# Kernel tuning notes

Hardware: AMD Instinct MI355X
Metric: run time of the kernel (lower is better)

## Reference

```python
import jax, jax.numpy as jnp
import numpy as np


def setup_inputs() -> dict:
    key = jax.random.key(0)
    k1, k2, k3 = jax.random.split(key, 3)
    l, p, m, n = 8, 1, 4096, 1024
    inp = jax.random.normal(k1, (l, p, m, n), dtype=jnp.float32)
    alpha = jax.random.uniform(k2, (1,), dtype=jnp.float32, minval=0.001, maxval=1.0)
    beta = jax.random.uniform(k3, (1,), dtype=jnp.float32, minval=0.001, maxval=1.0)
    return {"input": inp, "alpha": alpha, "beta": beta}


def reference(input, alpha, beta):
    # w[0] = 1; w[k] = w[k-1] + alpha / w[k-1] - beta * input[..., k-1]
    l, p, m, n = input.shape
    a = alpha[0]
    b = beta[0]
    # scan over the last axis: move it to leading axis; only first n-1 inputs drive the recurrence
    xs = jnp.moveaxis(input[..., : n - 1], -1, 0)  # (n-1, l, p, m)
    w0 = jnp.ones((l, p, m), dtype=input.dtype)

    def step(w, x):
        w_next = w + a / w - b * x
        return w_next, w_next

    _, ws = jax.lax.scan(step, w0, xs)  # (n-1, l, p, m)
    wm = jnp.concatenate([w0[None], ws], axis=0)  # (n, l, p, m)
    wm = jnp.moveaxis(wm, 0, -1)  # (l, p, m, n)
    return wm.reshape(l, m * n)  # valid because p == 1
```

## Files before the change

kernel.cpp:

```cpp
#include <hip/hip_runtime.h>


#define N_COLS 1024
#define CHUNK 16

__device__ __forceinline__ float stepf(float w, float x, float a, float b) {
    return __fsub_rn(__fadd_rn(w, __fdiv_rn(a, w)), __fmul_rn(b, x));
}

__device__ __forceinline__ void load_chunk(const float4* __restrict__ p, int j,
                                           float* __restrict__ x) {
#pragma unroll
    for (int q = 0; q < CHUNK / 4; ++q) {
        float4 t = p[j * (CHUNK / 4) + q];
        x[q * 4 + 0] = t.x;
        x[q * 4 + 1] = t.y;
        x[q * 4 + 2] = t.z;
        x[q * 4 + 3] = t.w;
    }
}

__device__ __forceinline__ void store_chunk(float4* __restrict__ p, int j,
                                            const float* __restrict__ o) {
#pragma unroll
    for (int q = 0; q < CHUNK / 4; ++q) {
        float4 t;
        t.x = o[q * 4 + 0];
        t.y = o[q * 4 + 1];
        t.z = o[q * 4 + 2];
        t.w = o[q * 4 + 3];
        p[j * (CHUNK / 4) + q] = t;
    }
}

__global__ __launch_bounds__(64) void DDK_77644418777662_kernel(
    const float* __restrict__ in, float* __restrict__ out,
    const float* __restrict__ alpha, const float* __restrict__ beta,
    int n_rows) {
    int row = blockIdx.x * 64 + threadIdx.x;
    if (row >= n_rows) return;

    const float a = alpha[0];
    const float b = beta[0];

    const float4* __restrict__ inr =
        reinterpret_cast<const float4*>(in + (size_t)row * N_COLS);
    float4* __restrict__ outr =
        reinterpret_cast<float4*>(out + (size_t)row * N_COLS);

    constexpr int NC = N_COLS / CHUNK;

    float x[CHUNK], xn[CHUNK], o[CHUNK];
    float w = 1.0f;

    load_chunk(inr, 0, x);

#pragma unroll 2
    for (int j = 0; j < NC; ++j) {
        if (j + 1 < NC) load_chunk(inr, j + 1, xn);

        o[0] = w;
#pragma unroll
        for (int i = 1; i < CHUNK; ++i) {
            w = stepf(w, x[i - 1], a, b);
            o[i] = w;
        }
        w = stepf(w, x[CHUNK - 1], a, b);

        store_chunk(outr, j, o);

#pragma unroll
        for (int i = 0; i < CHUNK; ++i) x[i] = xn[i];
    }
}

extern "C" void kernel_launch(void* const* d_in, const int* in_sizes, int n_in,
                              void* d_out, int out_size, void* d_ws, size_t ws_size,
                              hipStream_t stream) {
    const float* in = (const float*)d_in[0];
    const float* alpha = (const float*)d_in[1];
    const float* beta = (const float*)d_in[2];
    float* out = (float*)d_out;

    int total = in_sizes[0];
    int n_rows = total / N_COLS;

    dim3 grid((n_rows + 63) / 64);
    dim3 block(64);
    DDK_77644418777662_kernel<<<grid, block, 0, stream>>>(in, out, alpha, beta,
                                                          n_rows);
}
```

Baseline: 308.8 us.

## Stage input through LDS with async global_load_lds ring buffer and manual vmcnt waits

Replaces per-thread strided float4 global loads with a cooperative, coalesced global-to-LDS async copy (global_load_lds) into an 8-deep ring of chunk buffers. Each lane then reads its swizzled 16-element slice from LDS, while loads run 7 chunks ahead under hand-written s_waitcnt vmcnt counters. This targets the poor coalescing of row-per-thread reads and the latency exposure of the serial divide-bound recurrence. It relies on exact vmcnt bookkeeping, which also counts the output stores, and on no barrier being needed within a single wave. Any miscount would give a race.

```diff
diff --git a/kernel.cpp b/kernel.cpp
--- a/kernel.cpp
+++ b/kernel.cpp
@@ -2,76 +2,113 @@
 
 
 #define N_COLS 1024
-#define CHUNK 16
+#define NCHUNK 64
+#define NBUF 8
+
+#define WAITVM(n) asm volatile("s_waitcnt vmcnt(" #n ")" ::: "memory")
+#define WAITLGKM0() asm volatile("s_waitcnt lgkmcnt(0)" ::: "memory")
 
 __device__ __forceinline__ float stepf(float w, float x, float a, float b) {
     return __fsub_rn(__fadd_rn(w, __fdiv_rn(a, w)), __fmul_rn(b, x));
-}
-
-__device__ __forceinline__ void load_chunk(const float4* __restrict__ p, int j,
-                                           float* __restrict__ x) {
-#pragma unroll
-    for (int q = 0; q < CHUNK / 4; ++q) {
-        float4 t = p[j * (CHUNK / 4) + q];
-        x[q * 4 + 0] = t.x;
-        x[q * 4 + 1] = t.y;
-        x[q * 4 + 2] = t.z;
-        x[q * 4 + 3] = t.w;
-    }
-}
-
-__device__ __forceinline__ void store_chunk(float4* __restrict__ p, int j,
-                                            const float* __restrict__ o) {
-#pragma unroll
-    for (int q = 0; q < CHUNK / 4; ++q) {
-        float4 t;
-        t.x = o[q * 4 + 0];
-        t.y = o[q * 4 + 1];
-        t.z = o[q * 4 + 2];
-        t.w = o[q * 4 + 3];
-        p[j * (CHUNK / 4) + q] = t;
-    }
 }
 
 __global__ __launch_bounds__(64) void DDK_77644418777662_kernel(
     const float* __restrict__ in, float* __restrict__ out,
     const float* __restrict__ alpha, const float* __restrict__ beta,
     int n_rows) {
-    int row = blockIdx.x * 64 + threadIdx.x;
-    if (row >= n_rows) return;
+    __shared__ float lds[NBUF * 1024];
+
+    const int lane = threadIdx.x;
+    const int row_base = blockIdx.x * 64;
+    if (row_base >= n_rows) return;
 
     const float a = alpha[0];
     const float b = beta[0];
+    asm volatile("s_waitcnt vmcnt(0) lgkmcnt(0)" ::: "memory");
 
-    const float4* __restrict__ inr =
-        reinterpret_cast<const float4*>(in + (size_t)row * N_COLS);
-    float4* __restrict__ outr =
-        reinterpret_cast<float4*>(out + (size_t)row * N_COLS);
+    const int t = lane >> 2;
+    const int u = lane & 3;
+    const int c4 = u ^ ((t >> 1) & 3);
+    const float* pb0 = in + (size_t)(row_base + t) * N_COLS + c4 * 4;
+    const float* pb1 = pb0 + 16 * N_COLS;
+    const float* pb2 = pb0 + 32 * N_COLS;
+    const float* pb3 = pb0 + 48 * N_COLS;
 
-    constexpr int NC = N_COLS / CHUNK;
+    const int s2 = (lane >> 1) & 3;
+    const int sbase = 64 * (lane >> 4) + 4 * (lane & 15);
+    const int sl0 = (sbase + (0 ^ s2)) * 4;
+    const int sl1 = (sbase + (1 ^ s2)) * 4;
+    const int sl2 = (sbase + (2 ^ s2)) * 4;
+    const int sl3 = (sbase + (3 ^ s2)) * 4;
 
-    float x[CHUNK], xn[CHUNK], o[CHUNK];
+    float* outp = out + (size_t)(row_base + lane) * N_COLS;
+
+#define STAGE(c) do {                                                          \
+    float* dst_ = &lds[((c) & 7) * 1024];                                      \
+    __builtin_amdgcn_global_load_lds(                                          \
+        (const __attribute__((address_space(1))) void*)(pb0 + (c) * 16),       \
+        (__attribute__((address_space(3))) void*)(dst_ + 0), 16, 0, 0);        \
+    __builtin_amdgcn_global_load_lds(                                          \
+        (const __attribute__((address_space(1))) void*)(pb1 + (c) * 16),       \
+        (__attribute__((address_space(3))) void*)(dst_ + 256), 16, 0, 0);      \
+    __builtin_amdgcn_global_load_lds(                                          \
+        (const __attribute__((address_space(1))) void*)(pb2 + (c) * 16),       \
+        (__attribute__((address_space(3))) void*)(dst_ + 512), 16, 0, 0);      \
+    __builtin_amdgcn_global_load_lds(                                          \
+        (const __attribute__((address_space(1))) void*)(pb3 + (c) * 16),       \
+        (__attribute__((address_space(3))) void*)(dst_ + 768), 16, 0, 0);      \
+} while (0)
+
     float w = 1.0f;
 
-    load_chunk(inr, 0, x);
+#define BODY(c, DO_LOAD) do {                                                  \
+    const float* bufp_ = &lds[((c) & 7) * 1024];                               \
+    float4 xa_ = *(const float4*)(bufp_ + sl0);                                \
+    float4 xb_ = *(const float4*)(bufp_ + sl1);                                \
+    float4 xc_ = *(const float4*)(bufp_ + sl2);                                \
+    float4 xd_ = *(const float4*)(bufp_ + sl3);                                \
+    WAITLGKM0();                                                               \
+    if (DO_LOAD) STAGE((c) + 7);                                               \
+    float x_[16] = {xa_.x, xa_.y, xa_.z, xa_.w, xb_.x, xb_.y, xb_.z, xb_.w,    \
+                    xc_.x, xc_.y, xc_.z, xc_.w, xd_.x, xd_.y, xd_.z, xd_.w};   \
+    float o_[16];                                                              \
+    o_[0] = w;                                                                 \
+    _Pragma("unroll")                                                          \
+    for (int i_ = 1; i_ < 16; ++i_) { w = stepf(w, x_[i_ - 1], a, b); o_[i_] = w; } \
+    w = stepf(w, x_[15], a, b);                                                \
+    float4* op_ = (float4*)(outp + (c) * 16);                                  \
+    op_[0] = make_float4(o_[0], o_[1], o_[2], o_[3]);                          \
+    op_[1] = make_float4(o_[4], o_[5], o_[6], o_[7]);                          \
+    op_[2] = make_float4(o_[8], o_[9], o_[10], o_[11]);                        \
+    op_[3] = make_float4(o_[12], o_[13], o_[14], o_[15]);                      \
+} while (0)
 
-#pragma unroll 2
-    for (int j = 0; j < NC; ++j) {
-        if (j + 1 < NC) load_chunk(inr, j + 1, xn);
+    STAGE(0); STAGE(1); STAGE(2); STAGE(3); STAGE(4); STAGE(5); STAGE(6);
 
-        o[0] = w;
-#pragma unroll
-        for (int i = 1; i < CHUNK; ++i) {
-            w = stepf(w, x[i - 1], a, b);
-            o[i] = w;
-        }
-        w = stepf(w, x[CHUNK - 1], a, b);
+    WAITVM(24); BODY(0, 1);
+    WAITVM(28); BODY(1, 1);
+    WAITVM(32); BODY(2, 1);
+    WAITVM(36); BODY(3, 1);
+    WAITVM(40); BODY(4, 1);
+    WAITVM(44); BODY(5, 1);
+    WAITVM(48); BODY(6, 1);
 
-        store_chunk(outr, j, o);
+#pragma unroll 1
+    for (int c = 7; c <= 56; ++c) {
+        WAITVM(52);
+        BODY(c, 1);
+    }
 
-#pragma unroll
-        for (int i = 0; i < CHUNK; ++i) x[i] = xn[i];
-    }
+    WAITVM(52); BODY(57, 0);
+    WAITVM(48); BODY(58, 0);
+    WAITVM(44); BODY(59, 0);
+    WAITVM(40); BODY(60, 0);
+    WAITVM(36); BODY(61, 0);
+    WAITVM(32); BODY(62, 0);
+    WAITVM(28); BODY(63, 0);
+
+#undef BODY
+#undef STAGE
 }
 
 extern "C" void kernel_launch(void* const* d_in, const int* in_sizes, int n_in,
```

Measured after the change: 307.1 us. About the same (-0.6%).

## Warp-specialize recurrence kernel with async LDS loader, compute and store waves

Applied to the files above, without the earlier changes.

Restructures each 256-thread block into a loader wave that stages 16-column chunks for 128 rows into a 6-deep LDS ring via global_load_lds, two compute waves that run the sequential recurrence from LDS, and a store wave that drains a double-buffered LDS output to global memory. The goal is to overlap memory traffic with the latency-bound per-row recurrence and to get coalesced, swizzled row-chunk accesses. It also replaces the compiler division with hand-written inline asm for the IEEE-correct divide sequence. In exchange it adds a block barrier on every chunk, leaves half the waves without arithmetic, and assumes n_rows is a multiple of 128.

```diff
diff --git a/kernel.cpp b/kernel.cpp
--- a/kernel.cpp
+++ b/kernel.cpp
@@ -2,75 +2,157 @@
 
 
 #define N_COLS 1024
-#define CHUNK 16
+#define NCHUNK 64
+#define KIN 6
+
+#define WAITVM(n) asm volatile("s_waitcnt vmcnt(" #n ")" ::: "memory")
+#define WAITLGKM0() asm volatile("s_waitcnt lgkmcnt(0)" ::: "memory")
+#define BARRIER() __builtin_amdgcn_s_barrier()
+
+__device__ __forceinline__ float fdiv_rn_exact(float a, float w) {
+    float d, n, r0, e, r1, q, e2, q1, e3, f, res;
+    unsigned long long sj;
+    asm volatile(
+        "v_div_scale_f32 %[d], vcc, %[w], %[w], %[a]\n\t"
+        "v_div_scale_f32 %[n], %[sj], %[a], %[w], %[a]\n\t"
+        "v_rcp_f32 %[r0], %[d]\n\t"
+        "s_nop 1\n\t"
+        "v_fma_f32 %[e], -%[d], %[r0], 1.0\n\t"
+        "v_fma_f32 %[r1], %[e], %[r0], %[r0]\n\t"
+        "v_mul_f32 %[q], %[n], %[r1]\n\t"
+        "v_fma_f32 %[e2], -%[d], %[q], %[n]\n\t"
+        "v_fma_f32 %[q1], %[e2], %[r1], %[q]\n\t"
+        "v_fma_f32 %[e3], -%[d], %[q1], %[n]\n\t"
+        "v_div_fmas_f32 %[f], %[e3], %[r1], %[q1]\n\t"
+        "v_div_fixup_f32 %[res], %[f], %[w], %[a]"
+        : [d] "=&v"(d), [n] "=&v"(n), [r0] "=&v"(r0), [e] "=&v"(e),
+          [r1] "=&v"(r1), [q] "=&v"(q), [e2] "=&v"(e2), [q1] "=&v"(q1),
+          [e3] "=&v"(e3), [f] "=&v"(f), [res] "=v"(res), [sj] "=&s"(sj)
+        : [a] "v"(a), [w] "v"(w)
+        : "vcc");
+    return res;
+}
 
 __device__ __forceinline__ float stepf(float w, float x, float a, float b) {
-    return __fsub_rn(__fadd_rn(w, __fdiv_rn(a, w)), __fmul_rn(b, x));
+    return __fsub_rn(__fadd_rn(w, fdiv_rn_exact(a, w)), __fmul_rn(b, x));
 }
 
-__device__ __forceinline__ void load_chunk(const float4* __restrict__ p, int j,
-                                           float* __restrict__ x) {
-#pragma unroll
-    for (int q = 0; q < CHUNK / 4; ++q) {
-        float4 t = p[j * (CHUNK / 4) + q];
-        x[q * 4 + 0] = t.x;
-        x[q * 4 + 1] = t.y;
-        x[q * 4 + 2] = t.z;
-        x[q * 4 + 3] = t.w;
-    }
-}
-
-__device__ __forceinline__ void store_chunk(float4* __restrict__ p, int j,
-                                            const float* __restrict__ o) {
-#pragma unroll
-    for (int q = 0; q < CHUNK / 4; ++q) {
-        float4 t;
-        t.x = o[q * 4 + 0];
-        t.y = o[q * 4 + 1];
-        t.z = o[q * 4 + 2];
-        t.w = o[q * 4 + 3];
-        p[j * (CHUNK / 4) + q] = t;
-    }
-}
-
-__global__ __launch_bounds__(64) void DDK_77644418777662_kernel(
+__global__ __launch_bounds__(256) void DDK_77644418777662_kernel(
     const float* __restrict__ in, float* __restrict__ out,
     const float* __restrict__ alpha, const float* __restrict__ beta,
     int n_rows) {
-    int row = blockIdx.x * 64 + threadIdx.x;
-    if (row >= n_rows) return;
+    __shared__ float ibuf[KIN * 2048];
+    __shared__ float obuf[2 * 2048];
 
-    const float a = alpha[0];
-    const float b = beta[0];
+    const int tid = threadIdx.x;
+    const int wid = tid >> 6;
+    const int lane = tid & 63;
+    const int row_base = blockIdx.x * 128;
+    if (row_base >= n_rows) return;
 
-    const float4* __restrict__ inr =
-        reinterpret_cast<const float4*>(in + (size_t)row * N_COLS);
-    float4* __restrict__ outr =
-        reinterpret_cast<float4*>(out + (size_t)row * N_COLS);
+    const int t = lane >> 2;
+    const int u = lane & 3;
+    const int cg = u ^ ((t >> 1) & 3);
 
-    constexpr int NC = N_COLS / CHUNK;
+    if (wid == 2) {
+        const float* src0 = in + (size_t)(row_base + t) * N_COLS + cg * 4;
 
-    float x[CHUNK], xn[CHUNK], o[CHUNK];
-    float w = 1.0f;
+#define STAGE_AT(S, C) do {                                                    \
+    float* dst_ = ibuf + (S) * 2048;                                           \
+    const float* s_ = src0 + (size_t)(C) * 16;                                 \
+    _Pragma("unroll")                                                          \
+    for (int q_ = 0; q_ < 8; ++q_) {                                           \
+        __builtin_amdgcn_global_load_lds(                                      \
+            (const __attribute__((address_space(1))) void*)(s_ + q_ * 16 * N_COLS), \
+            (__attribute__((address_space(3))) void*)(dst_ + q_ * 256), 16, 0, 0);  \
+    }                                                                          \
+} while (0)
 
-    load_chunk(inr, 0, x);
+        WAITVM(0);
+        STAGE_AT(0, 0); STAGE_AT(1, 1); STAGE_AT(2, 2);
+        STAGE_AT(3, 3); STAGE_AT(4, 4);
+        WAITVM(32);
 
-#pragma unroll 2
-    for (int j = 0; j < NC; ++j) {
-        if (j + 1 < NC) load_chunk(inr, j + 1, xn);
+        int slot = KIN - 1;
+#pragma unroll 1
+        for (int c = 0; c < NCHUNK; ++c) {
+            BARRIER();
+            if (c <= NCHUNK - KIN) {
+                STAGE_AT(slot, c + KIN - 1);
+                WAITVM(32);
+                if (++slot == KIN) slot = 0;
+            } else if (c == 59) { WAITVM(24); }
+            else if (c == 60) { WAITVM(16); }
+            else if (c == 61) { WAITVM(8); }
+            else if (c == 62) { WAITVM(0); }
+        }
+        BARRIER();
+#undef STAGE_AT
 
-        o[0] = w;
+    } else if (wid == 3) {
+        float* dst0 = out + (size_t)(row_base + t) * N_COLS + cg * 4;
+
+#define STORE_CHUNK(C) do {                                                    \
+    const float* ob_ = obuf + ((C) & 1) * 2048;                                \
+    float4 v_[8];                                                              \
+    _Pragma("unroll")                                                          \
+    for (int q_ = 0; q_ < 8; ++q_)                                             \
+        v_[q_] = *(const float4*)(ob_ + q_ * 256 + lane * 4);                  \
+    WAITLGKM0();                                                               \
+    _Pragma("unroll")                                                          \
+    for (int q_ = 0; q_ < 8; ++q_)                                             \
+        *(float4*)(dst0 + (size_t)q_ * 16 * N_COLS + (size_t)(C) * 16) = v_[q_]; \
+} while (0)
+
+#pragma unroll 1
+        for (int c = 0; c < NCHUNK; ++c) {
+            BARRIER();
+            if (c >= 1) STORE_CHUNK(c - 1);
+        }
+        BARRIER();
+        STORE_CHUNK(NCHUNK - 1);
+#undef STORE_CHUNK
+
+    } else {
+        const float a = alpha[0];
+        const float b = beta[0];
+
+        const int r = (wid << 6) + lane;
+        const int rq = r >> 4, rr = r & 15;
+        const int s = (rr >> 1) & 3;
+        const int off0 = rq * 256 + (rr * 4 + (0 ^ s)) * 4;
+        const int off1 = rq * 256 + (rr * 4 + (1 ^ s)) * 4;
+        const int off2 = rq * 256 + (rr * 4 + (2 ^ s)) * 4;
+        const int off3 = rq * 256 + (rr * 4 + (3 ^ s)) * 4;
+
+        float w = 1.0f;
+        int rslot = 0;
+#pragma unroll 1
+        for (int c = 0; c < NCHUNK; ++c) {
+            BARRIER();
+            const float* ib = ibuf + rslot * 2048;
+            float4 xa = *(const float4*)(ib + off0);
+            float4 xb = *(const float4*)(ib + off1);
+            float4 xc = *(const float4*)(ib + off2);
+            float4 xd = *(const float4*)(ib + off3);
+            float x[16] = {xa.x, xa.y, xa.z, xa.w, xb.x, xb.y, xb.z, xb.w,
+                           xc.x, xc.y, xc.z, xc.w, xd.x, xd.y, xd.z, xd.w};
+            float o[16];
+            o[0] = w;
 #pragma unroll
-        for (int i = 1; i < CHUNK; ++i) {
-            w = stepf(w, x[i - 1], a, b);
-            o[i] = w;
+            for (int i = 1; i < 16; ++i) { w = stepf(w, x[i - 1], a, b); o[i] = w; }
+            w = stepf(w, x[15], a, b);
+
+            float* ob = obuf + (c & 1) * 2048;
+            *(float4*)(ob + off0) = make_float4(o[0], o[1], o[2], o[3]);
+            *(float4*)(ob + off1) = make_float4(o[4], o[5], o[6], o[7]);
+            *(float4*)(ob + off2) = make_float4(o[8], o[9], o[10], o[11]);
+            *(float4*)(ob + off3) = make_float4(o[12], o[13], o[14], o[15]);
+            WAITLGKM0();
+
+            if (++rslot == KIN) rslot = 0;
         }
-        w = stepf(w, x[CHUNK - 1], a, b);
-
-        store_chunk(outr, j, o);
-
-#pragma unroll
-        for (int i = 0; i < CHUNK; ++i) x[i] = xn[i];
+        BARRIER();
     }
 }
 
@@ -85,8 +167,8 @@
     int total = in_sizes[0];
     int n_rows = total / N_COLS;
 
-    dim3 grid((n_rows + 63) / 64);
-    dim3 block(64);
+    dim3 grid(n_rows / 128);
+    dim3 block(256);
     DDK_77644418777662_kernel<<<grid, block, 0, stream>>>(in, out, alpha, beta,
                                                           n_rows);
 }
```

Result: faster. 283.3 us (-8.2%).
